# Optimization experiments

Measured on AMD Instinct MI355X. Metric: run time of the kernel, lower is better.

## Reference

```python
import jax, jax.numpy as jnp
import numpy as np

SOC, EOS = 3, 2
NUM_HEADS = 12
LN_EPS = 1e-5


def setup_inputs() -> dict:
    key = jax.random.key(0)
    ks = jax.random.split(key, 24)
    B, S, D, N, FF, K = 8, 4096, 768, 1024, 3072, 640
    img = jax.random.normal(ks[0], (B, N, D), jnp.float32)
    hid = jax.random.normal(ks[1], (B, S, D), jnp.float32)
    seq = jax.random.randint(ks[2], (B, S), 4, 100)
    m = jax.random.uniform(ks[3], (B, S)) < 0.125
    seq = jnp.where(m, SOC, seq).at[:, 0].set(SOC)  # ensure >=1 SOC per row
    w = lambda k, a, b: jax.random.normal(k, (a, b), jnp.float32) * 0.02
    return {
        "img": img, "hid": hid, "seq": seq,
        "wq_s": w(ks[4], D, D), "wk_s": w(ks[5], D, D), "wv_s": w(ks[6], D, D), "wo_s": w(ks[7], D, D),
        "wq_c": w(ks[8], D, D), "wk_c": w(ks[9], D, D), "wv_c": w(ks[10], D, D), "wo_c": w(ks[11], D, D),
        "w_ff1": w(ks[12], D, FF), "w_ff2": w(ks[13], FF, D),
        "ln1_s": jnp.ones((D,)), "ln1_b": jnp.zeros((D,)),
        "ln2_s": jnp.ones((D,)), "ln2_b": jnp.zeros((D,)),
        "ln3_s": jnp.ones((D,)), "ln3_b": jnp.zeros((D,)),
        "cap": K,
    }


def _ln(x, s, b):
    mu = jnp.mean(x, axis=-1, keepdims=True)
    var = jnp.var(x, axis=-1, keepdims=True)
    return (x - mu) * jax.lax.rsqrt(var + LN_EPS) * s + b


def _mha(q_in, kv_in, wq, wk, wv, wo, key_mask):
    # q_in [B,Lq,D], kv_in [B,Lk,D], key_mask [B,Lk] bool or None
    B, Lq, D = q_in.shape
    H = NUM_HEADS
    dh = D // H
    q = (q_in @ wq).reshape(B, Lq, H, dh)
    k = (kv_in @ wk).reshape(B, -1, H, dh)
    v = (kv_in @ wv).reshape(B, -1, H, dh)
    scores = jnp.einsum("bqhd,bkhd->bhqk", q, k) / np.sqrt(dh).astype(q.dtype)
    if key_mask is not None:
        scores = jnp.where(key_mask[:, None, None, :], scores, jnp.asarray(-1e9, scores.dtype))
    att = jax.nn.softmax(scores, axis=-1)
    out = jnp.einsum("bhqk,bkhd->bqhd", att, v).reshape(B, Lq, D)
    return out @ wo


def _extract(data, mask, cap):
    # data [B,S,...], mask [B,S] bool -> packed+zero-padded [B,cap,...]
    pos = jnp.cumsum(mask, axis=1) - 1          # slot for each valid token
    pos = jnp.where(mask, pos, cap)             # invalid tokens -> dump slot
    def one(d, p):
        buf = jnp.zeros((cap + 1,) + d.shape[1:], d.dtype)
        return buf.at[p].set(d)[:cap]
        # note: dump slot cap is sliced away
    return jax.vmap(one)(data, pos), pos


def reference(img, hid, seq, wq_s, wk_s, wv_s, wo_s, wq_c, wk_c, wv_c, wo_c,
              w_ff1, w_ff2, ln1_s, ln1_b, ln2_s, ln2_b, ln3_s, ln3_b, cap):
    # mask: SOC tokens occurring before the first EOS
    soc = (seq == SOC) & (jnp.cumsum(seq == EOS, axis=1) == 0)  # [B,S]
    ext, pos = _extract(hid, soc, cap)                          # [B,K,D]
    counts = jnp.sum(soc, axis=1)                               # [B]
    run = jnp.arange(cap)[None, :] < counts[:, None]            # [B,K] valid slots

    # Blocks: pre-LN self-attn (key mask = run), cross-attn to img, FFN
    x = ext
    x = x + _mha(_ln(x, ln1_s, ln1_b), _ln(x, ln1_s, ln1_b), wq_s, wk_s, wv_s, wo_s, run)
    x = x + _mha(_ln(x, ln2_s, ln2_b), img, wq_c, wk_c, wv_c, wo_c, None)
    h = _ln(x, ln3_s, ln3_b)
    x = x + jax.nn.gelu(h @ w_ff1) @ w_ff2

    # masked_scatter back: each SOC position (b,s) takes x[b, pos[b,s]]
    idx = jnp.clip(pos, 0, cap - 1)
    gathered = jnp.take_along_axis(x, idx[:, :, None], axis=1)  # [B,S,D]
    hid_new = jnp.where(soc[:, :, None], gathered, hid)
    return hid_new, x
```

## Files before the change

### kernel.cpp

```cpp
#include <hip/hip_runtime.h>
#include <hip/hip_bf16.h>


#define B_    8
#define S_    4096
#define D_    768
#define N_    1024
#define FF_   3072
#define H_    12
#define DH_   64
#define KCAP  640
#define SOC_TOK 3
#define EOS_TOK 2

typedef __hip_bfloat16 bf16;
typedef unsigned short u16;
typedef __attribute__((ext_vector_type(8))) short short8;
typedef __attribute__((ext_vector_type(4))) float f32x4;

__device__ __forceinline__ u16 ftou16(float x){ union{bf16 b; u16 s;} c; c.b = __float2bfloat16(x); return c.s; }
__device__ __forceinline__ unsigned pk2(float lo, float hi){ return (unsigned)ftou16(lo) | ((unsigned)ftou16(hi)<<16); }

__device__ __forceinline__ f32x4 MFMA(short8 a, short8 b, f32x4 c){
  return __builtin_amdgcn_mfma_f32_16x16x32_bf16(a, b, c, 0, 0, 0);
}

__device__ __forceinline__ void gld16(const void* gp, void* lp){
  __builtin_amdgcn_global_load_lds(
    reinterpret_cast<const __attribute__((address_space(1))) unsigned int*>((size_t)gp),
    reinterpret_cast<__attribute__((address_space(3))) unsigned int*>((size_t)lp),
    16, 0, 0);
}

template<int N> __device__ __forceinline__ void vwait(){
  asm volatile("s_waitcnt vmcnt(%0)" :: "i"(N) : "memory");
}
__device__ __forceinline__ void wgbar(){ asm volatile("s_barrier" ::: "memory"); }

__device__ __forceinline__ int xcd_swz(){
  int id = blockIdx.x;
  return (id & 7) * ((int)gridDim.x >> 3) + (id >> 3);
}

__device__ void scan_body(const int* __restrict__ seq, int* __restrict__ pos,
                          int* __restrict__ src, int* __restrict__ counts, int b){
  int tid = threadIdx.x;
  __shared__ int sd[256];
  __shared__ int carryE, carryS;
  if (tid==0){ carryE=0; carryS=0; }
  __syncthreads();
  for (int c=0; c<S_; c+=256){
    int s   = c + tid;
    int tok = seq[b*S_ + s];
    int isE = (tok==EOS_TOK) ? 1 : 0;
    int isS = (tok==SOC_TOK) ? 1 : 0;
    sd[tid]=isE; __syncthreads();
    for (int off=1; off<256; off<<=1){ int t_=(tid>=off)?sd[tid-off]:0; __syncthreads(); sd[tid]+=t_; __syncthreads(); }
    int eIncl = sd[tid];
    int eTot  = sd[255];
    int valid = (isS && (carryE + eIncl)==0) ? 1 : 0;
    __syncthreads();
    sd[tid]=valid; __syncthreads();
    for (int off=1; off<256; off<<=1){ int t_=(tid>=off)?sd[tid-off]:0; __syncthreads(); sd[tid]+=t_; __syncthreads(); }
    int vIncl = sd[tid];
    int vTot  = sd[255];
    if (valid){
      int slot = carryS + vIncl - 1;
      pos[b*S_ + s] = slot;
      if (slot < KCAP) src[b*KCAP + slot] = s;
    } else {
      pos[b*S_ + s] = -1;
    }
    __syncthreads();
    if (tid==0){ carryE += eTot; carryS += vTot; }
    __syncthreads();
  }
  if (tid==0) counts[b] = (carryS < KCAP) ? carryS : KCAP;
}

struct TransArgs { const float* w[10]; u16* o[10]; };
__global__ __launch_bounds__(256) void transpose_scan_k(TransArgs a, const int* __restrict__ seq,
                                                        int* __restrict__ pos, int* __restrict__ src,
                                                        int* __restrict__ counts){
  int id = blockIdx.x;
  if (id >= 9216){ scan_body(seq, pos, src, counts, id - 9216); return; }
  __shared__ float tile[32][33];
  int wi, t, K, N;
  if (id < 4608){ wi = id/576; t = id%576; K = 768; N = 768; }
  else if (id < 6912){ wi = 8; t = id-4608; K = 768; N = 3072; }
  else { wi = 9; t = id-6912; K = 3072; N = 768; }
  const float* in = a.w[wi]; u16* out = a.o[wi];
  int nbx = N >> 5;
  int bx = t % nbx, by = t / nbx;
  int tx = threadIdx.x & 31, ty = threadIdx.x >> 5;
  #pragma unroll
  for (int i=0;i<4;++i)
    tile[ty + i*8][tx] = in[(size_t)(by*32 + ty + i*8)*N + bx*32 + tx];
  __syncthreads();
  #pragma unroll
  for (int i=0;i<4;++i)
    out[(size_t)(bx*32 + ty + i*8)*K + by*32 + tx] = ftou16(tile[tx][ty + i*8]);
}

__global__ __launch_bounds__(256) void gather_ln_k(const float* __restrict__ hid,
                                                   const int* __restrict__ src,
                                                   const int* __restrict__ counts,
                                                   const float* __restrict__ g, const float* __restrict__ bt,
                                                   float* __restrict__ X, u16* __restrict__ T0){
  int bk = blockIdx.x; int b = bk / KCAP; int k = bk % KCAP;
  int tid = threadIdx.x;
  float v0, v1, v2;
  if (k < counts[b]){
    const float* hr = hid + ((size_t)b*S_ + src[b*KCAP + k])*D_;
    v0 = hr[tid]; v1 = hr[tid+256]; v2 = hr[tid+512];
  } else { v0 = v1 = v2 = 0.f; }
  float* xr = X + (size_t)bk*D_;
  xr[tid] = v0; xr[tid+256] = v1; xr[tid+512] = v2;
  float s1=v0+v1+v2, s2=v0*v0+v1*v1+v2*v2;
  for (int off=32; off; off>>=1){ s1+=__shfl_xor(s1,off); s2+=__shfl_xor(s2,off); }
  __shared__ float red[8];
  __shared__ float mu_s, rs_s;
  int w=tid>>6, ln=tid&63;
  if (ln==0){ red[w]=s1; red[4+w]=s2; }
  __syncthreads();
  if (tid==0){
    float S1=red[0]+red[1]+red[2]+red[3];
    float S2=red[4]+red[5]+red[6]+red[7];
    float mu = S1*(1.f/D_);
    float var= S2*(1.f/D_) - mu*mu;
    mu_s=mu; rs_s=rsqrtf(var + 1e-5f);
  }
  __syncthreads();
  float mu=mu_s, rs=rs_s;
  u16* yr = T0 + (size_t)bk*D_;
  yr[tid]     = ftou16((v0-mu)*rs*g[tid]     + bt[tid]);
  yr[tid+256] = ftou16((v1-mu)*rs*g[tid+256] + bt[tid+256]);
  yr[tid+512] = ftou16((v2-mu)*rs*g[tid+512] + bt[tid+512]);
}

__global__ __launch_bounds__(256) void ln_k(const float* __restrict__ X, u16* __restrict__ Y,
                                            const float* __restrict__ g, const float* __restrict__ bt){
  int r = blockIdx.x; int tid = threadIdx.x;
  const float* xr = X + (size_t)r*D_;
  float v0=xr[tid], v1=xr[tid+256], v2=xr[tid+512];
  float s1=v0+v1+v2, s2=v0*v0+v1*v1+v2*v2;
  for (int off=32; off; off>>=1){ s1+=__shfl_xor(s1,off); s2+=__shfl_xor(s2,off); }
  __shared__ float red[8];
  __shared__ float mu_s, rs_s;
  int w=tid>>6, ln=tid&63;
  if (ln==0){ red[w]=s1; red[4+w]=s2; }
  __syncthreads();
  if (tid==0){
    float S1=red[0]+red[1]+red[2]+red[3];
    float S2=red[4]+red[5]+red[6]+red[7];
    float mu = S1*(1.f/D_);
    float var= S2*(1.f/D_) - mu*mu;
    mu_s=mu; rs_s=rsqrtf(var + 1e-5f);
  }
  __syncthreads();
  float mu=mu_s, rs=rs_s;
  u16* yr = Y + (size_t)r*D_;
  yr[tid]     = ftou16((v0-mu)*rs*g[tid]     + bt[tid]);
  yr[tid+256] = ftou16((v1-mu)*rs*g[tid+256] + bt[tid+256]);
  yr[tid+512] = ftou16((v2-mu)*rs*g[tid+512] + bt[tid+512]);
}

template<int MODE, typename TA>
__device__ __forceinline__ void gemm_body(char* ldsp, const TA* __restrict__ A, const u16* __restrict__ Bt,
                                          void* __restrict__ C0, void* __restrict__ C1, void* __restrict__ C2,
                                          int wgid, int N, int K){
  constexpr int BM = 64, MI = 2, LPS = 3;
  constexpr int NBUF = (sizeof(TA)==4) ? 2 : 3;
  u16* As = (u16*)ldsp;
  u16* Bs = (u16*)(ldsp + NBUF*(BM*32)*2);
  int nbx = N >> 7;
  int bx = wgid % nbx, by = wgid / nbx;
  int tid = threadIdx.x;
  int w = tid>>6, l = tid&63, g = l>>4, c = l&15;
  int wr = w&1, wc = w>>1;
  f32x4 acc[MI][4] = {};
  float4 rg0, rg1;
  const int NK = K/32;

  auto STAGEB = [&](int buf, int kt){
    #pragma unroll
    for (int p=0;p<2;++p){
      int row = w*32 + p*16 + (l>>2);
      int su  = (l&3) ^ ((row>>1)&3);
      gld16((const void*)(Bt + (size_t)(bx*128+row)*K + kt + su*8), (void*)&Bs[buf*128*32 + (w*32+p*16)*32]);
    }
  };
  auto STAGEA16 = [&](int buf, int kt){
    int row = w*16 + (l>>2);
    int su  = (l&3) ^ ((row>>1)&3);
    gld16((const void*)((const u16*)A + (size_t)(by*BM+row)*K + kt + su*8), (void*)&As[buf*BM*32 + (w*16)*32]);
  };
  auto LOADREG = [&](int kt){
    const float* ap = (const float*)A + (size_t)(by*BM + (tid>>2))*K + kt + (tid&3)*8;
    rg0 = *(const float4*)ap; rg1 = *(const float4*)(ap+4);
  };
  auto WRITEA = [&](int buf){
    int row = tid>>2, unit = tid&3;
    uint4 wv;
    wv.x=pk2(rg0.x,rg0.y); wv.y=pk2(rg0.z,rg0.w); wv.z=pk2(rg1.x,rg1.y); wv.w=pk2(rg1.z,rg1.w);
    int sw = (row>>1)&3;
    *(uint4*)&As[buf*BM*32 + row*32 + (unit^sw)*8] = wv;
  };
  auto COMPUTE = [&](int buf){
    short8 af[MI], bfr[4];
    #pragma unroll
    for (int mi=0;mi<MI;++mi){ int row = wr*32 + mi*16 + c; af[mi]  = *(const short8*)&As[buf*BM*32 + row*32 + (g^((row>>1)&3))*8]; }
    #pragma unroll
    for (int ni=0;ni<4;++ni){ int row = wc*64 + ni*16 + c;  bfr[ni] = *(const short8*)&Bs[buf*128*32 + row*32 + (g^((row>>1)&3))*8]; }
    #pragma unroll
    for (int mi=0;mi<MI;++mi)
      #pragma unroll
      for (int ni=0;ni<4;++ni) acc[mi][ni] = MFMA(af[mi], bfr[ni], acc[mi][ni]);
  };

  if constexpr (sizeof(TA)==4){
    LOADREG(0); STAGEB(0,0); WRITEA(0);
    __syncthreads();
    int buf = 0;
    for (int t=0;t<NK;++t){
      int ktn = (t+1)*32;
      if (t+1<NK){ LOADREG(ktn); STAGEB(buf^1, ktn); }
      COMPUTE(buf);
      if (t+1<NK) WRITEA(buf^1);
      __syncthreads();
      buf ^= 1;
    }
  } else {
    STAGEA16(0,0);  STAGEB(0,0);
    STAGEA16(1,32); STAGEB(1,32);
    vwait<LPS>();
    wgbar();
    int buf = 0;
    for (int t=0;t<NK;++t){
      if (t+2 < NK){
        int nb = buf+2; if (nb>=3) nb-=3;
        STAGEA16(nb,(t+2)*32); STAGEB(nb,(t+2)*32);
      }
      COMPUTE(buf);
      if (t < NK-2) vwait<LPS>(); else vwait<0>();
      wgbar();
      ++buf; if (buf==3) buf=0;
    }
  }

  int row0 = by*BM + wr*32, col0 = bx*128 + wc*64;
  #pragma unroll
  for (int mi=0;mi<MI;++mi)
    #pragma unroll
    for (int ni=0;ni<4;++ni)
      #pragma unroll
      for (int r=0;r<4;++r){
        int row = row0 + mi*16 + g*4 + r;
        int col = col0 + ni*16 + c;
        float v = acc[mi][ni][r];
        if (MODE==0){
          ((u16*)C0)[(size_t)row*N + col] = ftou16(v);
        } else if (MODE==1){
          ((float*)C0)[(size_t)row*N + col] += v;
        } else if (MODE==2){
          float z2 = 1.5957691216057308f*(v + 0.044715f*v*v*v);
          float e  = __expf(z2);
          float th = 1.f - 2.f/(e + 1.f);
          ((u16*)C0)[(size_t)row*N + col] = ftou16(0.5f*v*(1.f+th));
        } else if (MODE==6){
          size_t idx = (size_t)row*N + col;
          float fin = ((float*)C0)[idx] + v;
          ((float*)C0)[idx] = fin;
          ((float*)C1)[idx] = fin;
        } else if (MODE==4){
          if (col < 768)       ((u16*)C0)[(size_t)row*768 + col]       = ftou16(v);
          else if (col < 1536) ((u16*)C1)[(size_t)row*768 + col - 768] = ftou16(v);
          else {
            int vv = col - 1536; int bb = row / KCAP; int key = row - bb*KCAP;
            ((u16*)C2)[((size_t)(bb*768 + vv))*KCAP + key] = ftou16(v);
          }
        } else {
          if (col < 768) ((u16*)C0)[(size_t)row*768 + col] = ftou16(v);
          else {
            int vv = col - 768; int bb = row >> 10; int key = row & 1023;
            ((u16*)C2)[((size_t)(bb*768 + vv))*1024 + key] = ftou16(v);
          }
        }
      }
}

template<int MODE, typename TA>
__global__ __launch_bounds__(256) void gemm_k(const TA* __restrict__ A, const u16* __restrict__ Bt,
                                              void* __restrict__ C0, void* __restrict__ C1, void* __restrict__ C2,
                                              int N, int K){
  constexpr int LDSZ = ((sizeof(TA)==4)?2:3) * (64+128)*32*2;
  __shared__ __align__(16) char pool[LDSZ];
  gemm_body<MODE,TA>(pool, A, Bt, C0, C1, C2, xcd_swz(), N, K);
}

__global__ __launch_bounds__(256) void gemm_dual_k(const u16* __restrict__ T0, const u16* __restrict__ wq_ct,
                                                   u16* __restrict__ Qb,
                                                   const float* __restrict__ img, const u16* __restrict__ wkv_ct,
                                                   u16* __restrict__ Kb, u16* __restrict__ Vt){
  __shared__ __align__(16) char pool[3*(64+128)*32*2];
  int wgid = xcd_swz();
  if (wgid < 480) gemm_body<0,u16>  (pool, T0,  wq_ct,  Qb, nullptr, nullptr, wgid,      768,  768);
  else            gemm_body<5,float>(pool, img, wkv_ct, Kb, nullptr, Vt,      wgid-480, 1536,  768);
}

template<int MASKED>
__global__ __launch_bounds__(256) void attn_k(const u16* __restrict__ Q, const u16* __restrict__ Kb,
                                              const u16* __restrict__ Vt, u16* __restrict__ O,
                                              const int* __restrict__ counts, int Lk){
  __shared__ __align__(16) u16 Ks[3][64*64];
  __shared__ __align__(16) u16 Vs[3][64*64];
  __shared__ __align__(16) u16 P[4][16][72];
  int tid = threadIdx.x;
  int w = tid>>6, l = tid&63, g = l>>4, c = l&15;
  int wgid = xcd_swz();
  int qc = wgid % 5;
  int bh = wgid / 5;
  int h = bh % H_, b = bh / H_;
  int q0 = qc*128 + w*32;
  int cnt = MASKED ? counts[b] : Lk;
  int nt = (cnt + 63) >> 6;

  short8 qf[2][2];
  #pragma unroll
  for (int mi=0;mi<2;++mi){
    const u16* Qrow = Q + ((size_t)(b*KCAP + q0 + mi*16 + c))*D_ + h*DH_;
    qf[mi][0] = *(const short8*)(Qrow + g*8);
    qf[mi][1] = *(const short8*)(Qrow + 32 + g*8);
  }

  int srow8 = (l>>3);
  int sunit = l&7;
  auto STAGE = [&](int buf, int kb){
    #pragma unroll
    for (int p=0;p<2;++p){
      int r0 = w*16 + p*8;
      int rowK = r0 + srow8;
      int su = sunit ^ (rowK&7);
      gld16((const void*)(Kb + ((size_t)(b*Lk + kb + rowK))*D_ + h*DH_ + su*8), (void*)&Ks[buf][r0*64]);
      gld16((const void*)(Vt + ((size_t)(b*D_ + h*DH_ + rowK))*Lk + kb + su*8), (void*)&Vs[buf][r0*64]);
    }
  };

  f32x4 o[2][4] = {};
  float m_[2][4], l_[2][4] = {};
  #pragma unroll
  for (int mi=0;mi<2;++mi)
    #pragma unroll
    for (int r=0;r<4;++r) m_[mi][r] = -1e30f;

  STAGE(0, 0);
  if (nt > 1){ STAGE(1, 64); vwait<4>(); } else { vwait<0>(); }
  wgbar();
  int buf = 0;
  for (int t=0; t<nt; ++t){
    int kb = t*64;
    if (t+2 < nt){
      int nb = buf+2; if (nb>=3) nb-=3;
      STAGE(nb, kb+128);
    }
    short8 fr[4][2];
    #pragma unroll
    for (int nb=0;nb<4;++nb)
      #pragma unroll
      for (int kh=0;kh<2;++kh)
        fr[nb][kh] = *(const short8*)&Ks[buf][(nb*16+c)*64 + (((kh<<2)|g) ^ (c&7))*8];
    f32x4 z[2][4];
    #pragma unroll
    for (int mi=0;mi<2;++mi)
      #pragma unroll
      for (int nb=0;nb<4;++nb){
        f32x4 zz = {0.f,0.f,0.f,0.f};
        zz = MFMA(qf[mi][0], fr[nb][0], zz);
        zz = MFMA(qf[mi][1], fr[nb][1], zz);
        z[mi][nb] = zz;
      }
    float pv[2][4][4];
    #pragma unroll
    for (int nb=0;nb<4;++nb){
      bool msk = MASKED && (kb + nb*16 + c >= cnt);
      #pragma unroll
      for (int mi=0;mi<2;++mi)
        #pragma unroll
        for (int r=0;r<4;++r) pv[mi][nb][r] = msk ? -1e30f : z[mi][nb][r]*0.125f;
    }
    float scl[2][4];
    #pragma unroll
    for (int mi=0;mi<2;++mi){
      #pragma unroll
      for (int r=0;r<4;++r){
        float v = fmaxf(fmaxf(pv[mi][0][r],pv[mi][1][r]), fmaxf(pv[mi][2][r],pv[mi][3][r]));
        v = fmaxf(v, __shfl_xor(v,1)); v = fmaxf(v, __shfl_xor(v,2));
        v = fmaxf(v, __shfl_xor(v,4)); v = fmaxf(v, __shfl_xor(v,8));
        float nm = fmaxf(m_[mi][r], v);
        scl[mi][r] = __expf(m_[mi][r] - nm);
        m_[mi][r] = nm;
      }
      #pragma unroll
      for (int r=0;r<4;++r){
        float acc2 = 0.f;
        #pragma unroll
        for (int nb=0;nb<4;++nb){
          float e = __expf(pv[mi][nb][r] - m_[mi][r]);
          pv[mi][nb][r] = e; acc2 += e;
        }
        acc2 += __shfl_xor(acc2,1); acc2 += __shfl_xor(acc2,2);
        acc2 += __shfl_xor(acc2,4); acc2 += __shfl_xor(acc2,8);
        l_[mi][r] = l_[mi][r]*scl[mi][r] + acc2;
      }
      #pragma unroll
      for (int nbd=0;nbd<4;++nbd)
        #pragma unroll
        for (int r=0;r<4;++r) o[mi][nbd][r] *= scl[mi][r];
    }
    #pragma unroll
    for (int nbd=0;nbd<4;++nbd)
      #pragma unroll
      for (int kh=0;kh<2;++kh)
        fr[nbd][kh] = *(const short8*)&Vs[buf][(nbd*16+c)*64 + (((kh<<2)|g) ^ (c&7))*8];
    #pragma unroll
    for (int mi=0;mi<2;++mi){
      #pragma unroll
      for (int nb=0;nb<4;++nb)
        #pragma unroll
        for (int r=0;r<4;++r) P[w][g*4+r][nb*16+c] = ftou16(pv[mi][nb][r]);
      short8 pa0 = *(const short8*)&P[w][c][g*8];
      short8 pa1 = *(const short8*)&P[w][c][32 + g*8];
      #pragma unroll
      for (int nbd=0;nbd<4;++nbd){
        o[mi][nbd] = MFMA(pa0, fr[nbd][0], o[mi][nbd]);
        o[mi][nbd] = MFMA(pa1, fr[nbd][1], o[mi][nbd]);
      }
    }
    if (t < nt-2) vwait<4>(); else vwait<0>();
    wgbar();
    ++buf; if (buf==3) buf=0;
  }
  #pragma unroll
  for (int mi=0;mi<2;++mi)
    #pragma unroll
    for (int nbd=0;nbd<4;++nbd)
      #pragma unroll
      for (int r=0;r<4;++r)
        O[((size_t)(b*KCAP + q0 + mi*16 + g*4 + r))*D_ + h*DH_ + nbd*16 + c] = ftou16(o[mi][nbd][r] / l_[mi][r]);
}

__global__ __launch_bounds__(256) void scatter_k(const int* __restrict__ pos, const float* __restrict__ X,
                                                 const float* __restrict__ hid, float* __restrict__ out0){
  int bs = blockIdx.x; int tid = threadIdx.x;
  int b = bs >> 12;
  int p = pos[bs];
  float* orow = out0 + (size_t)bs*D_;
  if (p >= 0){
    int pc = p < KCAP ? p : (KCAP-1);
    const float* xr = X + ((size_t)(b*KCAP + pc))*D_;
    orow[tid]     = xr[tid];
    orow[tid+256] = xr[tid+256];
    orow[tid+512] = xr[tid+512];
  } else {
    const float* hr = hid + (size_t)bs*D_;
    orow[tid]     = hr[tid];
    orow[tid+256] = hr[tid+256];
    orow[tid+512] = hr[tid+512];
  }
}

extern "C" void kernel_launch(void* const* d_in, const int* in_sizes, int n_in,
                              void* d_out, int out_size, void* d_ws, size_t ws_size,
                              hipStream_t stream){
  const float* img  = (const float*)d_in[0];
  const float* hid  = (const float*)d_in[1];
  const int*   seq  = (const int*)  d_in[2];
  const float* W[10] = { (const float*)d_in[3], (const float*)d_in[4], (const float*)d_in[5], (const float*)d_in[6],
                         (const float*)d_in[7], (const float*)d_in[8], (const float*)d_in[9], (const float*)d_in[10],
                         (const float*)d_in[11], (const float*)d_in[12] };
  const float* ln1s = (const float*)d_in[13];
  const float* ln1b = (const float*)d_in[14];
  const float* ln2s = (const float*)d_in[15];
  const float* ln2b = (const float*)d_in[16];
  const float* ln3s = (const float*)d_in[17];
  const float* ln3b = (const float*)d_in[18];

  char* ws = (char*)d_ws;
  int*   pos    = (int*)  (ws + 0);
  int*   src    = (int*)  (ws + 131072);
  int*   counts = (int*)  (ws + 151552);
  float* X      = (float*)(ws + 151808);
  u16*   T0     = (u16*)  (ws + 15880448);
  u16*   Qb     = (u16*)  (ws + 23744768);
  u16*   Kb     = (u16*)  (ws + 31609088);
  u16*   Vt     = (u16*)  (ws + 44192000);
  u16*   AO     = (u16*)  (ws + 56774912);
  u16*   Wt     = (u16*)  (ws + 64639232);
  u16*   MID    = Qb;

  u16* wqkv_st = Wt + 0ull*589824;
  u16* wo_st   = Wt + 3ull*589824;
  u16* wq_ct   = Wt + 4ull*589824;
  u16* wkv_ct  = Wt + 5ull*589824;
  u16* wo_ct   = Wt + 7ull*589824;
  u16* wff1t   = Wt + 8ull*589824;
  u16* wff2t   = wff1t + 2359296;

  float* out0 = (float*)d_out;
  float* out1 = out0 + (size_t)B_*S_*D_;

  TransArgs ta;
  for (int i=0;i<10;++i) ta.w[i] = W[i];
  for (int i=0;i<8;++i)  ta.o[i] = Wt + (size_t)i*589824;
  ta.o[8] = wff1t; ta.o[9] = wff2t;

  transpose_scan_k<<<9224, 256, 0, stream>>>(ta, seq, pos, src, counts);
  gather_ln_k<<<B_*KCAP, 256, 0, stream>>>(hid, src, counts, ln1s, ln1b, X, T0);

  const int G_QKV  = (5120/64)*(2304/128);
  const int G_N768 = (5120/64)*(768/128);
  const int G_FF1  = (5120/64)*(3072/128);
  const int G_DUAL = 480 + (8192/64)*(1536/128);
  const int G_ATT  = B_*H_*5;

  gemm_k<4,u16><<<G_QKV, 256, 0, stream>>>(T0, wqkv_st, Qb, Kb, Vt, 2304, 768);
  attn_k<1><<<G_ATT, 256, 0, stream>>>(Qb, Kb, Vt, AO, counts, KCAP);
  gemm_k<1,u16><<<G_N768, 256, 0, stream>>>(AO, wo_st, X, nullptr, nullptr, 768, 768);

  ln_k<<<5120, 256, 0, stream>>>(X, T0, ln2s, ln2b);
  gemm_dual_k<<<G_DUAL, 256, 0, stream>>>(T0, wq_ct, Qb, img, wkv_ct, Kb, Vt);
  attn_k<0><<<G_ATT, 256, 0, stream>>>(Qb, Kb, Vt, AO, counts, N_);
  gemm_k<1,u16><<<G_N768, 256, 0, stream>>>(AO, wo_ct, X, nullptr, nullptr, 768, 768);

  ln_k<<<5120, 256, 0, stream>>>(X, T0, ln3s, ln3b);
  gemm_k<2,u16><<<G_FF1, 256, 0, stream>>>(T0, wff1t, MID, nullptr, nullptr, 3072, 768);
  gemm_k<6,u16><<<G_N768, 256, 0, stream>>>(MID, wff2t, X, out1, nullptr, 768, 3072);

  scatter_k<<<B_*S_, 256, 0, stream>>>(pos, X, hid, out0);
}
```

Measured before the change: 474.4 us.

## Add 128-row GEMM tiles and hoist cross-attn KV projection into self-attn QKV launch

Makes the GEMM body templated on the M tile size and adds a 128-row variant with double buffering. The image K/V projection for cross-attention does not depend on the block state, so it moves into one combined launch with the self-attention QKV GEMM, and the cross-attn Q projection becomes its own small GEMM. FF1 also switches to the 128-row tile. The aim is more data reuse per tile and fewer serialized launches, at the cost of more LDS and registers per block and separate workspace buffers for the self- and cross-attention K/V.

```diff
diff --git a/kernel.cpp b/kernel.cpp
--- a/kernel.cpp
+++ b/kernel.cpp
@@ -165,12 +165,12 @@
   yr[tid+512] = ftou16((v2-mu)*rs*g[tid+512] + bt[tid+512]);
 }
 
-template<int MODE, typename TA>
+template<int MODE, int BM, typename TA>
 __device__ __forceinline__ void gemm_body(char* ldsp, const TA* __restrict__ A, const u16* __restrict__ Bt,
                                           void* __restrict__ C0, void* __restrict__ C1, void* __restrict__ C2,
                                           int wgid, int N, int K){
-  constexpr int BM = 64, MI = 2, LPS = 3;
-  constexpr int NBUF = (sizeof(TA)==4) ? 2 : 3;
+  constexpr int MI   = BM/32;
+  constexpr int NBUF = (BM==128) ? 2 : ((sizeof(TA)==4) ? 2 : 3);
   u16* As = (u16*)ldsp;
   u16* Bs = (u16*)(ldsp + NBUF*(BM*32)*2);
   int nbx = N >> 7;
@@ -179,7 +179,7 @@
   int w = tid>>6, l = tid&63, g = l>>4, c = l&15;
   int wr = w&1, wc = w>>1;
   f32x4 acc[MI][4] = {};
-  float4 rg0, rg1;
+  float4 rg[4];
   const int NK = K/32;
 
   auto STAGEB = [&](int buf, int kt){
@@ -191,46 +191,78 @@
     }
   };
   auto STAGEA16 = [&](int buf, int kt){
-    int row = w*16 + (l>>2);
-    int su  = (l&3) ^ ((row>>1)&3);
-    gld16((const void*)((const u16*)A + (size_t)(by*BM+row)*K + kt + su*8), (void*)&As[buf*BM*32 + (w*16)*32]);
+    if constexpr (BM==128){
+      #pragma unroll
+      for (int p=0;p<2;++p){
+        int row = w*32 + p*16 + (l>>2);
+        int su  = (l&3) ^ ((row>>1)&3);
+        gld16((const void*)((const u16*)A + (size_t)(by*BM+row)*K + kt + su*8), (void*)&As[buf*BM*32 + (w*32+p*16)*32]);
+      }
+    } else {
+      int row = w*16 + (l>>2);
+      int su  = (l&3) ^ ((row>>1)&3);
+      gld16((const void*)((const u16*)A + (size_t)(by*BM+row)*K + kt + su*8), (void*)&As[buf*BM*32 + (w*16)*32]);
+    }
   };
   auto LOADREG = [&](int kt){
-    const float* ap = (const float*)A + (size_t)(by*BM + (tid>>2))*K + kt + (tid&3)*8;
-    rg0 = *(const float4*)ap; rg1 = *(const float4*)(ap+4);
+    if constexpr (BM==128){
+      const float* ap = (const float*)A + (size_t)(by*BM + (tid>>1))*K + kt + (tid&1)*16;
+      rg[0]=*(const float4*)ap;     rg[1]=*(const float4*)(ap+4);
+      rg[2]=*(const float4*)(ap+8); rg[3]=*(const float4*)(ap+12);
+    } else {
+      const float* ap = (const float*)A + (size_t)(by*BM + (tid>>2))*K + kt + (tid&3)*8;
+      rg[0] = *(const float4*)ap; rg[1] = *(const float4*)(ap+4);
+    }
   };
   auto WRITEA = [&](int buf){
-    int row = tid>>2, unit = tid&3;
-    uint4 wv;
-    wv.x=pk2(rg0.x,rg0.y); wv.y=pk2(rg0.z,rg0.w); wv.z=pk2(rg1.x,rg1.y); wv.w=pk2(rg1.z,rg1.w);
-    int sw = (row>>1)&3;
-    *(uint4*)&As[buf*BM*32 + row*32 + (unit^sw)*8] = wv;
+    if constexpr (BM==128){
+      int row = tid>>1, half = tid&1;
+      uint4 w0,w1;
+      w0.x=pk2(rg[0].x,rg[0].y); w0.y=pk2(rg[0].z,rg[0].w); w0.z=pk2(rg[1].x,rg[1].y); w0.w=pk2(rg[1].z,rg[1].w);
+      w1.x=pk2(rg[2].x,rg[2].y); w1.y=pk2(rg[2].z,rg[2].w); w1.z=pk2(rg[3].x,rg[3].y); w1.w=pk2(rg[3].z,rg[3].w);
+      int sw = (row>>1)&3;
+      *(uint4*)&As[buf*BM*32 + row*32 + ((half*2  )^sw)*8] = w0;
+      *(uint4*)&As[buf*BM*32 + row*32 + ((half*2+1)^sw)*8] = w1;
+    } else {
+      int row = tid>>2, unit = tid&3;
+      uint4 wv;
+      wv.x=pk2(rg[0].x,rg[0].y); wv.y=pk2(rg[0].z,rg[0].w); wv.z=pk2(rg[1].x,rg[1].y); wv.w=pk2(rg[1].z,rg[1].w);
+      int sw = (row>>1)&3;
+      *(uint4*)&As[buf*BM*32 + row*32 + (unit^sw)*8] = wv;
+    }
   };
   auto COMPUTE = [&](int buf){
     short8 af[MI], bfr[4];
     #pragma unroll
-    for (int mi=0;mi<MI;++mi){ int row = wr*32 + mi*16 + c; af[mi]  = *(const short8*)&As[buf*BM*32 + row*32 + (g^((row>>1)&3))*8]; }
-    #pragma unroll
-    for (int ni=0;ni<4;++ni){ int row = wc*64 + ni*16 + c;  bfr[ni] = *(const short8*)&Bs[buf*128*32 + row*32 + (g^((row>>1)&3))*8]; }
+    for (int mi=0;mi<MI;++mi){ int row = wr*(MI*16) + mi*16 + c; af[mi]  = *(const short8*)&As[buf*BM*32 + row*32 + (g^((row>>1)&3))*8]; }
+    #pragma unroll
+    for (int ni=0;ni<4;++ni){ int row = wc*64 + ni*16 + c;       bfr[ni] = *(const short8*)&Bs[buf*128*32 + row*32 + (g^((row>>1)&3))*8]; }
     #pragma unroll
     for (int mi=0;mi<MI;++mi)
       #pragma unroll
       for (int ni=0;ni<4;++ni) acc[mi][ni] = MFMA(af[mi], bfr[ni], acc[mi][ni]);
   };
 
-  if constexpr (sizeof(TA)==4){
-    LOADREG(0); STAGEB(0,0); WRITEA(0);
+  if constexpr (BM==128 || sizeof(TA)==4){
+    if constexpr (sizeof(TA)==4){ LOADREG(0); STAGEB(0,0); WRITEA(0); }
+    else { STAGEA16(0,0); STAGEB(0,0); }
     __syncthreads();
     int buf = 0;
     for (int t=0;t<NK;++t){
       int ktn = (t+1)*32;
-      if (t+1<NK){ LOADREG(ktn); STAGEB(buf^1, ktn); }
-      COMPUTE(buf);
-      if (t+1<NK) WRITEA(buf^1);
+      if constexpr (sizeof(TA)==4){
+        if (t+1<NK){ LOADREG(ktn); STAGEB(buf^1, ktn); }
+        COMPUTE(buf);
+        if (t+1<NK) WRITEA(buf^1);
+      } else {
+        if (t+1<NK){ STAGEA16(buf^1, ktn); STAGEB(buf^1, ktn); }
+        COMPUTE(buf);
+      }
       __syncthreads();
       buf ^= 1;
     }
   } else {
+    constexpr int LPS = 3;
     STAGEA16(0,0);  STAGEB(0,0);
     STAGEA16(1,32); STAGEB(1,32);
     vwait<LPS>();
@@ -248,7 +280,7 @@
     }
   }
 
-  int row0 = by*BM + wr*32, col0 = bx*128 + wc*64;
+  int row0 = by*BM + wr*(MI*16), col0 = bx*128 + wc*64;
   #pragma unroll
   for (int mi=0;mi<MI;++mi)
     #pragma unroll
@@ -289,23 +321,23 @@
       }
 }
 
-template<int MODE, typename TA>
+template<int MODE, int BM, typename TA>
 __global__ __launch_bounds__(256) void gemm_k(const TA* __restrict__ A, const u16* __restrict__ Bt,
                                               void* __restrict__ C0, void* __restrict__ C1, void* __restrict__ C2,
                                               int N, int K){
-  constexpr int LDSZ = ((sizeof(TA)==4)?2:3) * (64+128)*32*2;
-  __shared__ __align__(16) char pool[LDSZ];
-  gemm_body<MODE,TA>(pool, A, Bt, C0, C1, C2, xcd_swz(), N, K);
-}
-
-__global__ __launch_bounds__(256) void gemm_dual_k(const u16* __restrict__ T0, const u16* __restrict__ wq_ct,
-                                                   u16* __restrict__ Qb,
-                                                   const float* __restrict__ img, const u16* __restrict__ wkv_ct,
-                                                   u16* __restrict__ Kb, u16* __restrict__ Vt){
-  __shared__ __align__(16) char pool[3*(64+128)*32*2];
+  constexpr int NBUF = (BM==128) ? 2 : ((sizeof(TA)==4) ? 2 : 3);
+  __shared__ __align__(16) char pool[NBUF*(BM+128)*32*2];
+  gemm_body<MODE,BM,TA>(pool, A, Bt, C0, C1, C2, xcd_swz(), N, K);
+}
+
+__global__ __launch_bounds__(256) void mega1_k(const u16* __restrict__ T0, const u16* __restrict__ wqkv_st,
+                                               u16* __restrict__ Qb, u16* __restrict__ Kb, u16* __restrict__ VtS,
+                                               const float* __restrict__ img, const u16* __restrict__ wkv_ct,
+                                               u16* __restrict__ KbC, u16* __restrict__ VtC){
+  __shared__ __align__(16) char pool[2*(128+128)*32*2];
   int wgid = xcd_swz();
-  if (wgid < 480) gemm_body<0,u16>  (pool, T0,  wq_ct,  Qb, nullptr, nullptr, wgid,      768,  768);
-  else            gemm_body<5,float>(pool, img, wkv_ct, Kb, nullptr, Vt,      wgid-480, 1536,  768);
+  if (wgid < 720) gemm_body<4,128,u16>  (pool, T0,  wqkv_st, Qb,  Kb,      VtS, wgid,     2304, 768);
+  else            gemm_body<5,128,float>(pool, img, wkv_ct,  KbC, nullptr, VtC, wgid-720, 1536, 768);
 }
 
 template<int MASKED>
@@ -493,9 +525,11 @@
   u16*   T0     = (u16*)  (ws + 15880448);
   u16*   Qb     = (u16*)  (ws + 23744768);
   u16*   Kb     = (u16*)  (ws + 31609088);
-  u16*   Vt     = (u16*)  (ws + 44192000);
-  u16*   AO     = (u16*)  (ws + 56774912);
-  u16*   Wt     = (u16*)  (ws + 64639232);
+  u16*   VtS    = (u16*)  (ws + 39473408);
+  u16*   KbC    = (u16*)  (ws + 47337728);
+  u16*   VtC    = (u16*)  (ws + 59920640);
+  u16*   AO     = (u16*)  (ws + 72503552);
+  u16*   Wt     = (u16*)  (ws + 80367872);
   u16*   MID    = Qb;
 
   u16* wqkv_st = Wt + 0ull*589824;
@@ -517,24 +551,23 @@
   transpose_scan_k<<<9224, 256, 0, stream>>>(ta, seq, pos, src, counts);
   gather_ln_k<<<B_*KCAP, 256, 0, stream>>>(hid, src, counts, ln1s, ln1b, X, T0);
 
-  const int G_QKV  = (5120/64)*(2304/128);
-  const int G_N768 = (5120/64)*(768/128);
-  const int G_FF1  = (5120/64)*(3072/128);
-  const int G_DUAL = 480 + (8192/64)*(1536/128);
-  const int G_ATT  = B_*H_*5;
-
-  gemm_k<4,u16><<<G_QKV, 256, 0, stream>>>(T0, wqkv_st, Qb, Kb, Vt, 2304, 768);
-  attn_k<1><<<G_ATT, 256, 0, stream>>>(Qb, Kb, Vt, AO, counts, KCAP);
-  gemm_k<1,u16><<<G_N768, 256, 0, stream>>>(AO, wo_st, X, nullptr, nullptr, 768, 768);
+  const int G_MEGA1 = 720 + 768;
+  const int G_N768  = (5120/64)*(768/128);
+  const int G_FF1   = (5120/128)*(3072/128);
+  const int G_ATT   = B_*H_*5;
+
+  mega1_k<<<G_MEGA1, 256, 0, stream>>>(T0, wqkv_st, Qb, Kb, VtS, img, wkv_ct, KbC, VtC);
+  attn_k<1><<<G_ATT, 256, 0, stream>>>(Qb, Kb, VtS, AO, counts, KCAP);
+  gemm_k<1,64,u16><<<G_N768, 256, 0, stream>>>(AO, wo_st, X, nullptr, nullptr, 768, 768);
 
   ln_k<<<5120, 256, 0, stream>>>(X, T0, ln2s, ln2b);
-  gemm_dual_k<<<G_DUAL, 256, 0, stream>>>(T0, wq_ct, Qb, img, wkv_ct, Kb, Vt);
-  attn_k<0><<<G_ATT, 256, 0, stream>>>(Qb, Kb, Vt, AO, counts, N_);
-  gemm_k<1,u16><<<G_N768, 256, 0, stream>>>(AO, wo_ct, X, nullptr, nullptr, 768, 768);
+  gemm_k<0,64,u16><<<G_N768, 256, 0, stream>>>(T0, wq_ct, Qb, nullptr, nullptr, 768, 768);
+  attn_k<0><<<G_ATT, 256, 0, stream>>>(Qb, KbC, VtC, AO, counts, N_);
+  gemm_k<1,64,u16><<<G_N768, 256, 0, stream>>>(AO, wo_ct, X, nullptr, nullptr, 768, 768);
 
   ln_k<<<5120, 256, 0, stream>>>(X, T0, ln3s, ln3b);
-  gemm_k<2,u16><<<G_FF1, 256, 0, stream>>>(T0, wff1t, MID, nullptr, nullptr, 3072, 768);
-  gemm_k<6,u16><<<G_N768, 256, 0, stream>>>(MID, wff2t, X, out1, nullptr, 768, 3072);
+  gemm_k<2,128,u16><<<G_FF1, 256, 0, stream>>>(T0, wff1t, MID, nullptr, nullptr, 3072, 768);
+  gemm_k<6,64,u16><<<G_N768, 256, 0, stream>>>(MID, wff2t, X, out1, nullptr, 768, 3072);
 
   scatter_k<<<B_*S_, 256, 0, stream>>>(pos, X, hid, out0);
 }
```

Result: no change. 469.6 us (-1.0%).
